# Performance work log

Measured on AMD Instinct MI355X. Metric: run time of the kernel, lower is better.

The kernel has to match this reference:

```python
import jax, jax.numpy as jnp
import numpy as np

DIM = 768
GP_NUM = 49


def setup_inputs() -> dict:
    key = jax.random.key(0)
    ks = jax.random.split(key, 7)
    b, n, d = 16, 1024, DIM
    s = d ** -0.5
    x = jax.random.normal(ks[0], (b, n, d), dtype=jnp.float32)
    W_qkv = jax.random.normal(ks[1], (d, 3 * d), dtype=jnp.float32) * s
    b_qkv = jnp.zeros((3 * d,), dtype=jnp.float32)
    W_proj = jax.random.normal(ks[2], (d, d), dtype=jnp.float32) * s
    b_proj = jnp.zeros((d,), dtype=jnp.float32)
    W_gp = jax.random.normal(ks[3], (d, GP_NUM), dtype=jnp.float32) * s
    alpha = jnp.zeros((1,), dtype=jnp.float32)
    return {"x": x, "W_qkv": W_qkv, "b_qkv": b_qkv, "W_proj": W_proj,
            "b_proj": b_proj, "W_gp": W_gp, "alpha": alpha}


def reference(x, W_qkv, b_qkv, W_proj, b_proj, W_gp, alpha):
    d = x.shape[-1]
    scale = d ** -0.5
    qkv = x @ W_qkv + b_qkv                      # (b, n, 3d)
    q, k, v = jnp.split(qkv, 3, axis=-1)
    scores = jnp.einsum('bnd,bmd->bnm', q, k) * scale
    attn = jax.nn.softmax(scores, axis=-1)       # (b, n, n)
    gw = jax.nn.softmax(q @ W_gp, axis=-1)       # (b, n, gp_num)
    group = jnp.einsum('bng,bmg->bnm', gw, gw)   # (b, n, n)
    a = jax.nn.sigmoid(alpha)                    # (1,)
    weights = attn * (a + (1.0 - a) * group)
    out = jnp.einsum('bnm,bmd->bnd', weights, v)
    return out @ W_proj + b_proj
```

## Files before the change

kernel.cpp:

```cpp
#include <hip/hip_runtime.h>
#include <stdint.h>

typedef __attribute__((ext_vector_type(8))) short short8;
typedef __attribute__((ext_vector_type(4))) short short4v;
typedef __attribute__((ext_vector_type(4))) float floatx4;
typedef _Float16 half2v __attribute__((ext_vector_type(2)));

__device__ __forceinline__ float b2f(unsigned short u) {
  union { unsigned int i; float f; } v; v.i = ((unsigned int)u) << 16; return v.f;
}
__device__ __forceinline__ unsigned short f2b(float f) {
  union { float f; unsigned int i; } v; v.f = f;
  unsigned int i = v.i;
  return (unsigned short)((i + 0x7FFFu + ((i >> 16) & 1u)) >> 16);
}
__device__ __forceinline__ short4v pack4(float a, float b, float c, float d) {
  short4v r;
  r[0] = (short)f2b(a); r[1] = (short)f2b(b); r[2] = (short)f2b(c); r[3] = (short)f2b(d);
  return r;
}

__device__ __forceinline__ void stage16(const unsigned short* g, unsigned short* lds_base) {
  __builtin_amdgcn_global_load_lds((__attribute__((address_space(1))) const unsigned int*)g,
                                   (__attribute__((address_space(3))) unsigned int*)lds_base,
                                   16, 0, 0);
}

template<int SWZ>
__global__ __launch_bounds__(512, 2) void gemm256(
    const unsigned short* __restrict__ A, const unsigned short* __restrict__ B,
    unsigned short* __restrict__ Cb, float* __restrict__ Cf,
    const float* __restrict__ rowdiv, const float* __restrict__ bias,
    int K, int lda, int ldb, int ldc,
    long long sA, long long sB, long long sC, long long sRD)
{
  const int tid  = threadIdx.x;
  const int lane = tid & 63;
  const int wave = tid >> 6;
  const int wr = wave >> 2;
  const int wc = wave & 3;
  int m0, n0;
  if (SWZ > 0) {
    const int lin  = blockIdx.x;
    const int xcd  = lin & 7;
    const int rem  = lin >> 3;
    const int yloc = rem / 9;
    const int x    = rem - yloc * 9;
    m0 = (xcd * SWZ + yloc) * 256;
    n0 = x * 256;
  } else {
    m0 = blockIdx.y * 256;
    n0 = blockIdx.x * 256;
  }
  const int bz = blockIdx.z;
  A += (long long)bz * sA;
  B += (long long)bz * sB;
  const float* rd = rowdiv ? rowdiv + (long long)bz * sRD : (const float*)0;

  __shared__ __align__(16) unsigned short lds[3 * 16384];

  floatx4 acc[8][4];
#pragma unroll
  for (int i = 0; i < 8; ++i)
#pragma unroll
    for (int j = 0; j < 4; ++j) acc[i][j] = floatx4{0.f, 0.f, 0.f, 0.f};

  const int t    = (lane & 7) ^ (lane >> 3);
  const int srow = 2 * (lane >> 3) + (t >> 2);
  const int scol = (t & 3) * 8;
  const unsigned short* ga0 = A + (long long)(m0 + wave * 32 + srow) * lda + scol;
  const unsigned short* ga1 = ga0 + 16LL * lda;
  const unsigned short* gb0 = B + (long long)(n0 + wave * 32 + srow) * ldb + scol;
  const unsigned short* gb1 = gb0 + 16LL * ldb;

  const int l15  = lane & 15;
  const int q    = lane >> 4;
  const int rofs = (l15 >> 1) * 64 + (((q + 4 * (l15 & 1)) ^ (l15 >> 1)) * 8);

  short8 af[4], bfv[4];

  auto STAGE_A = [&](int kt, int buf) {
    unsigned short* d = lds + buf * 16384 + wave * 1024;
    stage16(ga0 + kt, d);
    stage16(ga1 + kt, d + 512);
  };
  auto STAGE_B = [&](int kt, int buf) {
    unsigned short* d = lds + buf * 16384 + 8192 + wave * 1024;
    stage16(gb0 + kt, d);
    stage16(gb1 + kt, d + 512);
  };
  auto READ_A = [&](int buf, int base) {
    const unsigned short* Ab = lds + buf * 16384;
#pragma unroll
    for (int i = 0; i < 4; ++i)
      af[i] = *(const short8*)&Ab[(wr * 64 + (base + i) * 8) * 64 + rofs];
  };
  auto READ_B = [&](int buf) {
    const unsigned short* Bb = lds + buf * 16384 + 8192;
#pragma unroll
    for (int j = 0; j < 4; ++j)
      bfv[j] = *(const short8*)&Bb[(wc * 32 + j * 8) * 64 + rofs];
  };
  auto MFMA_BLK = [&](int h) {
#pragma unroll
    for (int i = 0; i < 4; ++i)
#pragma unroll
      for (int j = 0; j < 4; ++j)
        acc[h * 4 + i][j] = __builtin_amdgcn_mfma_f32_16x16x32_bf16(bfv[j], af[i], acc[h * 4 + i][j], 0, 0, 0);
  };

  const int nt = K >> 5;
  int cur = 0;

  STAGE_A(0, 0);  STAGE_B(0, 0);
  STAGE_A(32, 1); STAGE_B(32, 1);
  asm volatile("s_waitcnt vmcnt(4)" ::: "memory");
  __builtin_amdgcn_s_barrier();

  for (int tt = 0; tt < nt - 2; ++tt) {
    const int nb  = (cur == 0) ? 2 : cur - 1;
    const int kt2 = (tt + 2) << 5;
    READ_B(cur);
    READ_A(cur, 0);
    STAGE_A(kt2, nb);
    __builtin_amdgcn_s_barrier();
    __builtin_amdgcn_s_setprio(1);
    MFMA_BLK(0);
    __builtin_amdgcn_s_setprio(0);
    __builtin_amdgcn_s_barrier();
    READ_A(cur, 4);
    STAGE_B(kt2, nb);
    __builtin_amdgcn_s_barrier();
    __builtin_amdgcn_s_setprio(1);
    MFMA_BLK(1);
    __builtin_amdgcn_s_setprio(0);
    asm volatile("s_waitcnt vmcnt(4)" ::: "memory");
    __builtin_amdgcn_s_barrier();
    cur = (cur == 2) ? 0 : cur + 1;
  }
  {
    READ_B(cur);
    READ_A(cur, 0);
    __builtin_amdgcn_s_barrier();
    __builtin_amdgcn_s_setprio(1);
    MFMA_BLK(0);
    __builtin_amdgcn_s_setprio(0);
    __builtin_amdgcn_s_barrier();
    READ_A(cur, 4);
    __builtin_amdgcn_s_setprio(1);
    MFMA_BLK(1);
    __builtin_amdgcn_s_setprio(0);
    asm volatile("s_waitcnt vmcnt(0)" ::: "memory");
    __builtin_amdgcn_s_barrier();
    cur = (cur == 2) ? 0 : cur + 1;
  }
  {
    READ_B(cur);
    READ_A(cur, 0);
    __builtin_amdgcn_s_barrier();
    __builtin_amdgcn_s_setprio(1);
    MFMA_BLK(0);
    __builtin_amdgcn_s_setprio(0);
    READ_A(cur, 4);
    __builtin_amdgcn_s_setprio(1);
    MFMA_BLK(1);
    __builtin_amdgcn_s_setprio(0);
  }

#pragma unroll
  for (int i = 0; i < 8; ++i) {
    const int row = m0 + wr * 128 + i * 16 + l15;
    const float rcp = rd ? __builtin_amdgcn_rcpf(rd[row]) : 1.0f;
#pragma unroll
    for (int j = 0; j < 4; ++j) {
      const int colb = n0 + wc * 64 + j * 16 + q * 4;
      floatx4 v = acc[i][j];
      if (rd) { v[0] *= rcp; v[1] *= rcp; v[2] *= rcp; v[3] *= rcp; }
      if (bias) {
        const float4 bi = *(const float4*)&bias[colb];
        v[0] += bi.x; v[1] += bi.y; v[2] += bi.z; v[3] += bi.w;
      }
      if (Cb) *(short4v*)&Cb[(long long)bz * sC + (long long)row * ldc + colb] = pack4(v[0], v[1], v[2], v[3]);
      else    *(floatx4*)&Cf[(long long)bz * sC + (long long)row * ldc + colb] = v;
    }
  }
}

__global__ __launch_bounds__(256) void score_weights(
    const unsigned short* __restrict__ qkv, const unsigned short* __restrict__ gw,
    unsigned short* __restrict__ Wout, float* __restrict__ L,
    const float* __restrict__ alpha)
{
  const int tid  = threadIdx.x;
  const int lane = tid & 63;
  const int wave = tid >> 6;
  const int wr = wave >> 1, wc = wave & 1;
  const int n0 = blockIdx.x * 128;
  const int m0 = blockIdx.y * 128;
  const int b  = blockIdx.z;

  const int l15 = lane & 15;
  const int q   = lane >> 4;
  const int q8  = q * 8;

  const unsigned short* gq = gw + ((long long)(b * 1024 + m0 + wr * 64)) * 64;
  const unsigned short* gk = gw + ((long long)(b * 1024 + n0 + wc * 64)) * 64;
  floatx4 gacc[4][4];
#pragma unroll
  for (int i = 0; i < 4; ++i)
#pragma unroll
    for (int j = 0; j < 4; ++j) gacc[i][j] = floatx4{0.f, 0.f, 0.f, 0.f};
#pragma unroll
  for (int ks = 0; ks < 2; ++ks) {
    short8 af[4], bfv[4];
#pragma unroll
    for (int i = 0; i < 4; ++i) af[i]  = *(const short8*)&gq[(long long)(i * 16 + l15) * 64 + ks * 32 + q8];
#pragma unroll
    for (int j = 0; j < 4; ++j) bfv[j] = *(const short8*)&gk[(long long)(j * 16 + l15) * 64 + ks * 32 + q8];
#pragma unroll
    for (int i = 0; i < 4; ++i)
#pragma unroll
      for (int j = 0; j < 4; ++j)
        gacc[i][j] = __builtin_amdgcn_mfma_f32_16x16x32_bf16(bfv[j], af[i], gacc[i][j], 0, 0, 0);
  }
  const float aa    = 1.0f / (1.0f + __expf(-alpha[0]));
  const float onema = 1.0f - aa;
  half2v gfp[4][4][2];
#pragma unroll
  for (int i = 0; i < 4; ++i)
#pragma unroll
    for (int j = 0; j < 4; ++j) {
      gfp[i][j][0] = half2v{(_Float16)(aa + onema * gacc[i][j][0]),
                            (_Float16)(aa + onema * gacc[i][j][1])};
      gfp[i][j][1] = half2v{(_Float16)(aa + onema * gacc[i][j][2]),
                            (_Float16)(aa + onema * gacc[i][j][3])};
    }

  const unsigned short* Aq = qkv + ((long long)(b * 1024 + m0)) * 2304;
  const unsigned short* Bk = qkv + ((long long)(b * 1024 + n0)) * 2304 + 768;

  __shared__ unsigned short As[128 * 32];
  __shared__ unsigned short Bs[128 * 32];

  floatx4 sacc[4][4];
#pragma unroll
  for (int i = 0; i < 4; ++i)
#pragma unroll
    for (int j = 0; j < 4; ++j) sacc[i][j] = floatx4{0.f, 0.f, 0.f, 0.f};

  const int t    = (lane & 7) ^ (lane >> 3);
  const int srow = 2 * (lane >> 3) + (t >> 2);
  const int scol = (t & 3) * 8;
  const unsigned short* ga0 = Aq + (long long)(wave * 32 + srow) * 2304 + scol;
  const unsigned short* ga1 = ga0 + 16LL * 2304;
  const unsigned short* gb0 = Bk + (long long)(wave * 32 + srow) * 2304 + scol;
  const unsigned short* gb1 = gb0 + 16LL * 2304;
  unsigned short* lA0 = As + wave * 1024;
  unsigned short* lA1 = lA0 + 512;
  unsigned short* lB0 = Bs + wave * 1024;
  unsigned short* lB1 = lB0 + 512;

  const int rofs = (l15 >> 1) * 64 + (((q + 4 * (l15 & 1)) ^ (l15 >> 1)) * 8);

  for (int kt = 0; kt < 768; kt += 32) {
    __syncthreads();
    stage16(ga0 + kt, lA0);
    stage16(ga1 + kt, lA1);
    stage16(gb0 + kt, lB0);
    stage16(gb1 + kt, lB1);
    __syncthreads();
    short8 af[4], bfv[4];
#pragma unroll
    for (int i = 0; i < 4; ++i) af[i]  = *(const short8*)&As[(wr * 32 + i * 8) * 64 + rofs];
#pragma unroll
    for (int j = 0; j < 4; ++j) bfv[j] = *(const short8*)&Bs[(wc * 32 + j * 8) * 64 + rofs];
#pragma unroll
    for (int i = 0; i < 4; ++i)
#pragma unroll
      for (int j = 0; j < 4; ++j)
        sacc[i][j] = __builtin_amdgcn_mfma_f32_16x16x32_bf16(bfv[j], af[i], sacc[i][j], 0, 0, 0);
  }

  const float scale = 0.03608439182435161f;
  unsigned short* Wb = Wout + ((long long)b << 20);

#pragma unroll
  for (int i = 0; i < 4; ++i) {
    const int row = m0 + wr * 64 + i * 16 + l15;
    float ls = 0.0f;
#pragma unroll
    for (int j = 0; j < 4; ++j) {
      const int colb = n0 + wc * 64 + j * 16 + q * 4;
      float e0 = __expf(sacc[i][j][0] * scale);
      float e1 = __expf(sacc[i][j][1] * scale);
      float e2 = __expf(sacc[i][j][2] * scale);
      float e3 = __expf(sacc[i][j][3] * scale);
      ls += (e0 + e1) + (e2 + e3);
      *(short4v*)&Wb[(long long)row * 1024 + colb] =
        pack4(e0 * (float)gfp[i][j][0][0], e1 * (float)gfp[i][j][0][1],
              e2 * (float)gfp[i][j][1][0], e3 * (float)gfp[i][j][1][1]);
    }
    ls += __shfl_xor(ls, 16, 64);
    ls += __shfl_xor(ls, 32, 64);
    if (lane < 16) atomicAdd(&L[b * 1024 + row], ls);
  }
}

__global__ __launch_bounds__(256) void gw_mfma(
    const unsigned short* __restrict__ qkv, const unsigned short* __restrict__ Wgp64,
    unsigned short* __restrict__ gw)
{
  const int lane = threadIdx.x & 63;
  const int wave = threadIdx.x >> 6;
  const int l15  = lane & 15;
  const int q    = lane >> 4;
  const int q8   = q * 8;
  const long long row0 = (long long)blockIdx.x * 64 + wave * 16;
  const unsigned short* A = qkv + row0 * 2304;

  floatx4 acc[4];
#pragma unroll
  for (int j = 0; j < 4; ++j) acc[j] = floatx4{0.f, 0.f, 0.f, 0.f};

  for (int kt = 0; kt < 768; kt += 32) {
    short8 af = *(const short8*)&A[(long long)l15 * 2304 + kt + q8];
    short8 bf[4];
#pragma unroll
    for (int j = 0; j < 4; ++j)
      bf[j] = *(const short8*)&Wgp64[(j * 16 + l15) * 768 + kt + q8];
#pragma unroll
    for (int j = 0; j < 4; ++j)
      acc[j] = __builtin_amdgcn_mfma_f32_16x16x32_bf16(bf[j], af, acc[j], 0, 0, 0);
  }

  float mx = -1e30f;
#pragma unroll
  for (int j = 0; j < 4; ++j)
#pragma unroll
    for (int e = 0; e < 4; ++e) {
      const int col = j * 16 + q * 4 + e;
      if (col < 49) mx = fmaxf(mx, acc[j][e]);
    }
  mx = fmaxf(mx, __shfl_xor(mx, 16, 64));
  mx = fmaxf(mx, __shfl_xor(mx, 32, 64));

  float ev[4][4];
  float s = 0.0f;
#pragma unroll
  for (int j = 0; j < 4; ++j)
#pragma unroll
    for (int e = 0; e < 4; ++e) {
      const int col = j * 16 + q * 4 + e;
      const float x = (col < 49) ? __expf(acc[j][e] - mx) : 0.0f;
      ev[j][e] = x;
      s += x;
    }
  s += __shfl_xor(s, 16, 64);
  s += __shfl_xor(s, 32, 64);
  const float inv = 1.0f / s;

  unsigned short* out = gw + (row0 + l15) * 64;
#pragma unroll
  for (int j = 0; j < 4; ++j)
    *(short4v*)&out[j * 16 + q * 4] =
      pack4(ev[j][0] * inv, ev[j][1] * inv, ev[j][2] * inv, ev[j][3] * inv);
}

__global__ void convert_f2b(const float* __restrict__ in, unsigned short* __restrict__ out, long long n)
{
  long long i = ((long long)blockIdx.x * 256 + threadIdx.x) * 4;
  if (i + 3 >= n) {
    for (long long k = i; k < n; ++k) out[k] = f2b(in[k]);
    return;
  }
  float4 v = *(const float4*)(in + i);
  out[i + 0] = f2b(v.x);
  out[i + 1] = f2b(v.y);
  out[i + 2] = f2b(v.z);
  out[i + 3] = f2b(v.w);
}

__global__ void transpose_f2b(const float* __restrict__ in, unsigned short* __restrict__ out,
                              int R, int C, int ldin, int ldout)
{
  __shared__ unsigned short t[32][33];
  const int c0 = blockIdx.x * 32, r0 = blockIdx.y * 32;
  for (int i = threadIdx.y; i < 32; i += 8) {
    const int r = r0 + i, c = c0 + threadIdx.x;
    if (r < R && c < C) t[i][threadIdx.x] = f2b(in[(long long)r * ldin + c]);
  }
  __syncthreads();
  for (int i = threadIdx.y; i < 32; i += 8) {
    const int r = c0 + i, c = r0 + threadIdx.x;
    if (r < C && c < R) out[(long long)r * ldout + c] = t[threadIdx.x][i];
  }
}

extern "C" void kernel_launch(void* const* d_in, const int* in_sizes, int n_in,
                              void* d_out, int out_size, void* d_ws, size_t ws_size,
                              hipStream_t stream)
{
  const float* x      = (const float*)d_in[0];
  const float* W_qkv  = (const float*)d_in[1];
  const float* b_qkv  = (const float*)d_in[2];
  const float* W_proj = (const float*)d_in[3];
  const float* b_proj = (const float*)d_in[4];
  const float* W_gp   = (const float*)d_in[5];
  const float* alpha  = (const float*)d_in[6];

  char* p = (char*)d_ws;
  auto alloc = [&](size_t bytes) { char* r = p; p += (bytes + 255) & ~255ULL; return r; };
  unsigned short* qkv    = (unsigned short*)alloc(16384ULL * 2304 * 2);
  unsigned short* xb     = (unsigned short*)alloc(16384ULL * 768 * 2);
  unsigned short* WqkvT  = (unsigned short*)alloc(2304ULL * 768 * 2);
  unsigned short* WprojT = (unsigned short*)alloc(768ULL * 768 * 2);
  unsigned short* Wgp64  = (unsigned short*)alloc(64ULL * 768 * 2);
  unsigned short* gwbuf  = (unsigned short*)alloc(16384ULL * 64 * 2);
  float*          Lbuf   = (float*)alloc(16384ULL * 4);
  unsigned short* wmat   = (unsigned short*)alloc(16ULL * 1024 * 1024 * 2);
  unsigned short* vpT    = (unsigned short*)alloc(16ULL * 768 * 1024 * 2);

  const dim3 blk256(256);
  const dim3 blk512(512);
  const dim3 tb(32, 8);

  convert_f2b<<<dim3(12288), blk256, 0, stream>>>(x, xb, 16384LL * 768);
  transpose_f2b<<<dim3(72, 24), tb, 0, stream>>>(W_qkv, WqkvT, 768, 2304, 2304, 768);
  transpose_f2b<<<dim3(24, 24), tb, 0, stream>>>(W_proj, WprojT, 768, 768, 768, 768);
  hipMemsetAsync(Wgp64, 0, 64ULL * 768 * 2, stream);
  transpose_f2b<<<dim3(2, 24), tb, 0, stream>>>(W_gp, Wgp64, 768, 49, 49, 768);

  gemm256<8><<<dim3(576, 1, 1), blk512, 0, stream>>>(xb, WqkvT, qkv, (float*)0,
                                                     (const float*)0, b_qkv,
                                                     768, 768, 768, 2304, 0, 0, 0, 0);

  gw_mfma<<<dim3(256), blk256, 0, stream>>>(qkv, Wgp64, gwbuf);

  hipMemsetAsync(Lbuf, 0, 16384 * 4, stream);

  score_weights<<<dim3(8, 8, 16), blk256, 0, stream>>>(qkv, gwbuf, wmat, Lbuf, alpha);

  gemm256<0><<<dim3(4, 3, 16), blk512, 0, stream>>>(WprojT, qkv + 1536, vpT, (float*)0,
                                                    (const float*)0, (const float*)0,
                                                    768, 768, 2304, 1024,
                                                    0, 1024LL * 2304, 768LL * 1024, 0);

  gemm256<0><<<dim3(3, 4, 16), blk512, 0, stream>>>(wmat, vpT, (unsigned short*)0, (float*)d_out,
                                                    Lbuf, b_proj,
                                                    1024, 1024, 1024, 768,
                                                    1024LL * 1024, 768LL * 1024, 1024LL * 768, 1024);
}
```

Baseline: 370.3 us.

## Fold V projection into output projection via combined weight matrix

The V slice of the QKV GEMM is no longer computed. A combined weight W_proj^T·W_v is precomputed once per call, and vpT is produced directly from x with that matrix. The V bias is folded into the output bias through a small bias kernel, which relies on the softmax-normalised weights summing to one. This removes a third of the QKV GEMM and the V writes, at the cost of a few extra small kernels and a change in rounding order.

```diff
diff --git a/kernel.cpp b/kernel.cpp
--- a/kernel.cpp
+++ b/kernel.cpp
@@ -26,7 +26,7 @@
                                    16, 0, 0);
 }
 
-template<int SWZ>
+template<int SWZ, int NXT>
 __global__ __launch_bounds__(512, 2) void gemm256(
     const unsigned short* __restrict__ A, const unsigned short* __restrict__ B,
     unsigned short* __restrict__ Cb, float* __restrict__ Cf,
@@ -40,12 +40,12 @@
   const int wr = wave >> 2;
   const int wc = wave & 3;
   int m0, n0;
-  if (SWZ > 0) {
+  if constexpr (SWZ > 0) {
     const int lin  = blockIdx.x;
     const int xcd  = lin & 7;
     const int rem  = lin >> 3;
-    const int yloc = rem / 9;
-    const int x    = rem - yloc * 9;
+    const int yloc = rem / NXT;
+    const int x    = rem - yloc * NXT;
     m0 = (xcd * SWZ + yloc) * 256;
     n0 = x * 256;
   } else {
@@ -236,8 +236,8 @@
                             (_Float16)(aa + onema * gacc[i][j][3])};
     }
 
-  const unsigned short* Aq = qkv + ((long long)(b * 1024 + m0)) * 2304;
-  const unsigned short* Bk = qkv + ((long long)(b * 1024 + n0)) * 2304 + 768;
+  const unsigned short* Aq = qkv + ((long long)(b * 1024 + m0)) * 1536;
+  const unsigned short* Bk = qkv + ((long long)(b * 1024 + n0)) * 1536 + 768;
 
   __shared__ unsigned short As[128 * 32];
   __shared__ unsigned short Bs[128 * 32];
@@ -251,10 +251,10 @@
   const int t    = (lane & 7) ^ (lane >> 3);
   const int srow = 2 * (lane >> 3) + (t >> 2);
   const int scol = (t & 3) * 8;
-  const unsigned short* ga0 = Aq + (long long)(wave * 32 + srow) * 2304 + scol;
-  const unsigned short* ga1 = ga0 + 16LL * 2304;
-  const unsigned short* gb0 = Bk + (long long)(wave * 32 + srow) * 2304 + scol;
-  const unsigned short* gb1 = gb0 + 16LL * 2304;
+  const unsigned short* ga0 = Aq + (long long)(wave * 32 + srow) * 1536 + scol;
+  const unsigned short* ga1 = ga0 + 16LL * 1536;
+  const unsigned short* gb0 = Bk + (long long)(wave * 32 + srow) * 1536 + scol;
+  const unsigned short* gb1 = gb0 + 16LL * 1536;
   unsigned short* lA0 = As + wave * 1024;
   unsigned short* lA1 = lA0 + 512;
   unsigned short* lB0 = Bs + wave * 1024;
@@ -316,14 +316,14 @@
   const int q    = lane >> 4;
   const int q8   = q * 8;
   const long long row0 = (long long)blockIdx.x * 64 + wave * 16;
-  const unsigned short* A = qkv + row0 * 2304;
+  const unsigned short* A = qkv + row0 * 1536;
 
   floatx4 acc[4];
 #pragma unroll
   for (int j = 0; j < 4; ++j) acc[j] = floatx4{0.f, 0.f, 0.f, 0.f};
 
   for (int kt = 0; kt < 768; kt += 32) {
-    short8 af = *(const short8*)&A[(long long)l15 * 2304 + kt + q8];
+    short8 af = *(const short8*)&A[(long long)l15 * 1536 + kt + q8];
     short8 bf[4];
 #pragma unroll
     for (int j = 0; j < 4; ++j)
@@ -396,6 +396,25 @@
   }
 }
 
+__global__ void slice_f2b(const float* __restrict__ in, unsigned short* __restrict__ out)
+{
+  const long long idx = (long long)blockIdx.x * 256 + threadIdx.x;
+  const int r = (int)(idx / 768), c = (int)(idx - (long long)r * 768);
+  out[idx] = f2b(in[(long long)r * 2304 + 1536 + c]);
+}
+
+__global__ __launch_bounds__(256) void bias2_kernel(
+    const float* __restrict__ W_proj, const float* __restrict__ b_qkv,
+    const float* __restrict__ b_proj, float* __restrict__ bias2)
+{
+  const int j = blockIdx.x * 256 + threadIdx.x;
+  if (j >= 768) return;
+  float s = b_proj[j];
+#pragma unroll 4
+  for (int d = 0; d < 768; ++d) s += W_proj[d * 768 + j] * b_qkv[1536 + d];
+  bias2[j] = s;
+}
+
 extern "C" void kernel_launch(void* const* d_in, const int* in_sizes, int n_in,
                               void* d_out, int out_size, void* d_ws, size_t ws_size,
                               hipStream_t stream)
@@ -410,13 +429,16 @@
 
   char* p = (char*)d_ws;
   auto alloc = [&](size_t bytes) { char* r = p; p += (bytes + 255) & ~255ULL; return r; };
-  unsigned short* qkv    = (unsigned short*)alloc(16384ULL * 2304 * 2);
+  unsigned short* qk     = (unsigned short*)alloc(16384ULL * 1536 * 2);
   unsigned short* xb     = (unsigned short*)alloc(16384ULL * 768 * 2);
-  unsigned short* WqkvT  = (unsigned short*)alloc(2304ULL * 768 * 2);
+  unsigned short* WqkvT  = (unsigned short*)alloc(1536ULL * 768 * 2);
   unsigned short* WprojT = (unsigned short*)alloc(768ULL * 768 * 2);
+  unsigned short* WvB    = (unsigned short*)alloc(768ULL * 768 * 2);
+  unsigned short* Wcomb  = (unsigned short*)alloc(768ULL * 768 * 2);
   unsigned short* Wgp64  = (unsigned short*)alloc(64ULL * 768 * 2);
   unsigned short* gwbuf  = (unsigned short*)alloc(16384ULL * 64 * 2);
   float*          Lbuf   = (float*)alloc(16384ULL * 4);
+  float*          bias2  = (float*)alloc(768ULL * 4);
   unsigned short* wmat   = (unsigned short*)alloc(16ULL * 1024 * 1024 * 2);
   unsigned short* vpT    = (unsigned short*)alloc(16ULL * 768 * 1024 * 2);
 
@@ -425,28 +447,34 @@
   const dim3 tb(32, 8);
 
   convert_f2b<<<dim3(12288), blk256, 0, stream>>>(x, xb, 16384LL * 768);
-  transpose_f2b<<<dim3(72, 24), tb, 0, stream>>>(W_qkv, WqkvT, 768, 2304, 2304, 768);
+  transpose_f2b<<<dim3(48, 24), tb, 0, stream>>>(W_qkv, WqkvT, 768, 1536, 2304, 768);
   transpose_f2b<<<dim3(24, 24), tb, 0, stream>>>(W_proj, WprojT, 768, 768, 768, 768);
   hipMemsetAsync(Wgp64, 0, 64ULL * 768 * 2, stream);
   transpose_f2b<<<dim3(2, 24), tb, 0, stream>>>(W_gp, Wgp64, 768, 49, 49, 768);
-
-  gemm256<8><<<dim3(576, 1, 1), blk512, 0, stream>>>(xb, WqkvT, qkv, (float*)0,
-                                                     (const float*)0, b_qkv,
-                                                     768, 768, 768, 2304, 0, 0, 0, 0);
-
-  gw_mfma<<<dim3(256), blk256, 0, stream>>>(qkv, Wgp64, gwbuf);
+  slice_f2b<<<dim3(2304), blk256, 0, stream>>>(W_qkv, WvB);
+
+  gemm256<0, 1><<<dim3(3, 3, 1), blk512, 0, stream>>>(WprojT, WvB, Wcomb, (float*)0,
+                                                      (const float*)0, (const float*)0,
+                                                      768, 768, 768, 768, 0, 0, 0, 0);
+  bias2_kernel<<<dim3(3), blk256, 0, stream>>>(W_proj, b_qkv, b_proj, bias2);
+
+  gemm256<8, 6><<<dim3(384, 1, 1), blk512, 0, stream>>>(xb, WqkvT, qk, (float*)0,
+                                                        (const float*)0, b_qkv,
+                                                        768, 768, 768, 1536, 0, 0, 0, 0);
+
+  gw_mfma<<<dim3(256), blk256, 0, stream>>>(qk, Wgp64, gwbuf);
 
   hipMemsetAsync(Lbuf, 0, 16384 * 4, stream);
 
-  score_weights<<<dim3(8, 8, 16), blk256, 0, stream>>>(qkv, gwbuf, wmat, Lbuf, alpha);
-
-  gemm256<0><<<dim3(4, 3, 16), blk512, 0, stream>>>(WprojT, qkv + 1536, vpT, (float*)0,
-                                                    (const float*)0, (const float*)0,
-                                                    768, 768, 2304, 1024,
-                                                    0, 1024LL * 2304, 768LL * 1024, 0);
-
-  gemm256<0><<<dim3(3, 4, 16), blk512, 0, stream>>>(wmat, vpT, (unsigned short*)0, (float*)d_out,
-                                                    Lbuf, b_proj,
-                                                    1024, 1024, 1024, 768,
-                                                    1024LL * 1024, 768LL * 1024, 1024LL * 768, 1024);
-}
+  score_weights<<<dim3(8, 8, 16), blk256, 0, stream>>>(qk, gwbuf, wmat, Lbuf, alpha);
+
+  gemm256<0, 1><<<dim3(4, 3, 16), blk512, 0, stream>>>(Wcomb, xb, vpT, (float*)0,
+                                                       (const float*)0, (const float*)0,
+                                                       768, 768, 768, 1024,
+                                                       0, 1024LL * 768, 768LL * 1024, 0);
+
+  gemm256<0, 1><<<dim3(3, 4, 16), blk512, 0, stream>>>(wmat, vpT, (unsigned short*)0, (float*)d_out,
+                                                       Lbuf, bias2,
+                                                       1024, 1024, 1024, 768,
+                                                       1024LL * 1024, 768LL * 1024, 1024LL * 768, 1024);
+}
```

Result: slower. 432.4 us (+16.8%).
